# Performance work log

Measured on AMD Instinct MI355X. Metric: run time of the kernel, lower is better.

The kernel has to match this reference:

```python
import jax, jax.numpy as jnp
import numpy as np

HEADS = 8
DIM_HEAD = 64


def setup_inputs() -> dict:
    key = jax.random.key(0)
    k1, k2, k3 = jax.random.split(key, 3)
    B, F, N_PATCH, DIM = 8, 16, 196, 512
    seq = 1 + F * N_PATCH  # 3137
    inner = HEADS * DIM_HEAD  # 512
    x = jax.random.normal(k1, (B, seq, DIM), dtype=jnp.float32)
    Wqkv = jax.random.normal(k2, (DIM, 3 * inner), dtype=jnp.float32) * (DIM ** -0.5)
    Wout = jax.random.normal(k3, (inner, DIM), dtype=jnp.float32) * (inner ** -0.5)
    bout = jnp.zeros((DIM,), dtype=jnp.float32)
    return {"x": x, "Wqkv": Wqkv, "Wout": Wout, "bout": bout, "f": F}


def _attn(q, k, v):
    # q: [b, i, d], k/v: [b, j, d]
    sim = jnp.einsum('bid,bjd->bij', q, k)
    a = jax.nn.softmax(sim, axis=-1)
    return jnp.einsum('bij,bjd->bid', a, v)


def reference(x, Wqkv, Wout, bout, f):
    B, N, D = x.shape
    h, dh = HEADS, DIM_HEAD
    scale = dh ** -0.5
    qkv = x @ Wqkv  # [B, N, 3*h*dh]
    q, k, v = jnp.split(qkv, 3, axis=-1)

    def to_bh(t):  # 'b n (h d) -> (b h) n d'
        return t.reshape(B, N, h, dh).transpose(0, 2, 1, 3).reshape(B * h, N, dh)

    q, k, v = to_bh(q), to_bh(k), to_bh(v)
    q = q * scale

    cls_q, q_ = q[:, :1], q[:, 1:]
    cls_k, k_ = k[:, :1], k[:, 1:]
    cls_v, v_ = v[:, :1], v[:, 1:]

    # cls token attends to all tokens
    cls_out = _attn(cls_q, k, v)  # [(b h), 1, dh]

    n = (N - 1) // f
    # 'b (f n) d -> (b f) n d'
    def split_frames(t):
        return t.reshape(B * h, f, n, dh).reshape(B * h * f, n, dh)

    q_, k_, v_ = split_frames(q_), split_frames(k_), split_frames(v_)

    # 'b () d -> (b r) () d' with r = f
    cls_k = jnp.repeat(cls_k, f, axis=0)
    cls_v = jnp.repeat(cls_v, f, axis=0)
    k_ = jnp.concatenate((cls_k, k_), axis=1)  # [(b h f), n+1, dh]
    v_ = jnp.concatenate((cls_v, v_), axis=1)

    out = _attn(q_, k_, v_)  # [(b h f), n, dh]
    out = out.reshape(B * h, f * n, dh)  # '(b f) n d -> b (f n) d'
    out = jnp.concatenate((cls_out, out), axis=1)  # [(b h), N, dh]
    # '(b h) n d -> b n (h d)'
    out = out.reshape(B, h, N, dh).transpose(0, 2, 1, 3).reshape(B, N, h * dh)
    return out @ Wout + bout
```

## Files before the change

kernel.cpp:

```cpp
#include <hip/hip_runtime.h>
#include <hip/hip_bf16.h>

#define B_    8
#define F_    16
#define NP_   196
#define SEQ_  3137
#define H_    8
#define DH_   64
#define BH_   64
#define M_    25096
#define MPAD_ 25216
#define DIM_  512
#define NQKV_ 1536
#define NCH_  13

typedef _Float16 half8_t __attribute__((ext_vector_type(8)));
typedef _Float16 half4_t __attribute__((ext_vector_type(4)));
typedef float f32x4 __attribute__((ext_vector_type(4)));

#define XH_OFF     ((size_t)0)
#define WQKVT_OFF  ((size_t)25821184)
#define WOUTT_OFF  ((size_t)27394048)
#define QH_OFF     ((size_t)27918336)
#define KH_OFF     ((size_t)53616640)
#define VH_OFF     ((size_t)79314944)
#define ATTNH_OFF  ((size_t)105013248)
#define CLSP_OFF   XH_OFF

__device__ __forceinline__ void load_lds16(const _Float16* g, _Float16* l) {
  __builtin_amdgcn_global_load_lds(
      (const __attribute__((address_space(1))) void*)g,
      (__attribute__((address_space(3))) void*)l, 16, 0, 0);
}

__device__ __forceinline__ int xcd_swz(int orig, int nwg) {
  int q = nwg >> 3, r = nwg & 7;
  int x = orig & 7, j = orig >> 3;
  return (x < r ? x * (q + 1) : r * (q + 1) + (x - r) * q) + j;
}

__global__ __launch_bounds__(256) void convert_x_kernel(
    const float* __restrict__ x, _Float16* __restrict__ xh) {
  const size_t n8 = (size_t)M_ * DIM_ / 8;
  for (size_t i = (size_t)blockIdx.x * blockDim.x + threadIdx.x; i < n8;
       i += (size_t)gridDim.x * blockDim.x) {
    float4 a = ((const float4*)x)[2 * i];
    float4 b = ((const float4*)x)[2 * i + 1];
    half8_t h;
    h[0] = (_Float16)a.x; h[1] = (_Float16)a.y; h[2] = (_Float16)a.z; h[3] = (_Float16)a.w;
    h[4] = (_Float16)b.x; h[5] = (_Float16)b.y; h[6] = (_Float16)b.z; h[7] = (_Float16)b.w;
    ((half8_t*)xh)[i] = h;
  }
}

__global__ __launch_bounds__(256) void transpose_conv2_kernel(
    const float* __restrict__ wqkv, _Float16* __restrict__ wqkvT,
    const float* __restrict__ wout, _Float16* __restrict__ woutT) {
  __shared__ float tile[32][33];
  int by = blockIdx.y;
  const float* in; _Float16* out; int C;
  if (by < 48) { in = wqkv; out = wqkvT; C = NQKV_; }
  else         { in = wout; out = woutT; C = DIM_;  by -= 48; }
  const int r0 = blockIdx.x * 32, c0 = by * 32;
  const int lr = threadIdx.x >> 5, lc = threadIdx.x & 31;
#pragma unroll
  for (int p = 0; p < 4; ++p) {
    int r = p * 8 + lr;
    tile[r][lc] = in[(size_t)(r0 + r) * C + c0 + lc];
  }
  __syncthreads();
#pragma unroll
  for (int p = 0; p < 4; ++p) {
    int rr = p * 8 + lr;
    out[(size_t)(c0 + rr) * DIM_ + r0 + lc] = (_Float16)tile[lc][rr];
  }
}

__device__ __forceinline__ void gemm_mainloop_f16(
    const _Float16* __restrict__ A, const _Float16* __restrict__ Bt,
    int m0, int n0, _Float16* As, _Float16* Bs, f32x4 acc[4][4]) {
  const int tid = threadIdx.x;
  const int w = tid >> 6, lane = tid & 63;
  const int wr = w >> 1, wc = w & 1;
  const int lrow = lane & 15;
  const int g = lane >> 4;
  const int sw = lane & 7;

  const int srow = lane >> 3;
  const int scol = ((lane & 7) ^ srow) << 3;

  for (int k0 = 0; k0 < DIM_; k0 += 64) {
#pragma unroll
    for (int i = 0; i < 4; ++i) {
      int c = w * 4 + i;
      int r = c * 8 + srow;
      load_lds16(A + (size_t)(m0 + r) * DIM_ + k0 + scol, As + c * 512);
      load_lds16(Bt + (size_t)(n0 + r) * DIM_ + k0 + scol, Bs + c * 512);
    }
    __syncthreads();

#pragma unroll
    for (int kk = 0; kk < 2; ++kk) {
      const int kf = ((kk * 4 + g) ^ sw) << 3;
      half8_t a[4], b[4];
#pragma unroll
      for (int m = 0; m < 4; ++m)
        a[m] = *(const half8_t*)(As + (wr * 64 + m * 16 + lrow) * 64 + kf);
#pragma unroll
      for (int n = 0; n < 4; ++n)
        b[n] = *(const half8_t*)(Bs + (wc * 64 + n * 16 + lrow) * 64 + kf);
#pragma unroll
      for (int m = 0; m < 4; ++m)
#pragma unroll
        for (int n = 0; n < 4; ++n)
          acc[m][n] = __builtin_amdgcn_mfma_f32_16x16x32_f16(a[m], b[n], acc[m][n], 0, 0, 0);
    }
    __syncthreads();
  }
}

__global__ __launch_bounds__(256) void qkv_gemm_kernel(
    const _Float16* __restrict__ xh, const _Float16* __restrict__ wqkvT,
    _Float16* __restrict__ qh, _Float16* __restrict__ kh, _Float16* __restrict__ vh) {
  __shared__ _Float16 As[128 * 64];
  __shared__ _Float16 Bs[128 * 64];
  const int nwg = 197 * 12;
  const int lin = xcd_swz(blockIdx.x, nwg);
  const int mb = lin / 12, nb = lin - mb * 12;
  const int m0 = mb * 128, n0 = nb * 128;

  f32x4 acc[4][4];
#pragma unroll
  for (int m = 0; m < 4; ++m)
#pragma unroll
    for (int n = 0; n < 4; ++n) acc[m][n] = (f32x4)0.f;

  gemm_mainloop_f16(xh, wqkvT, m0, n0, As, Bs, acc);

  const int tid = threadIdx.x;
  const int w = tid >> 6, lane = tid & 63;
  const int wr = w >> 1, wc = w & 1;
  const int g = lane >> 4, lrow = lane & 15;

  _Float16* stg = (w < 2) ? (As + w * 4096) : (Bs + (w - 2) * 4096);
  const int gcb0 = n0 + wc * 64;
  const int which = gcb0 >> 9;
  const int h = (gcb0 >> 6) & 7;
  const float scale = (which == 0) ? 0.125f : 1.0f;
  _Float16* dst = (which == 0) ? qh : (which == 1) ? kh : vh;

#pragma unroll
  for (int m = 0; m < 4; ++m)
#pragma unroll
    for (int n = 0; n < 4; ++n)
#pragma unroll
      for (int j = 0; j < 4; ++j) {
        int row = m * 16 + g * 4 + j;
        int col = n * 16 + lrow;
        int slot = (col >> 3) ^ (row & 7);
        stg[row * 64 + slot * 8 + (col & 7)] = (_Float16)(acc[m][n][j] * scale);
      }
  asm volatile("s_waitcnt lgkmcnt(0)" ::: "memory");
  __builtin_amdgcn_sched_barrier(0);

  const int rl = lane >> 3, cs = lane & 7;
#pragma unroll
  for (int rr = 0; rr < 8; ++rr) {
    int row = rr * 8 + rl;
    int grow = m0 + wr * 64 + row;
    if (grow < M_) {
      int b = grow / SEQ_;
      int t = grow - b * SEQ_;
      half8_t v = *(const half8_t*)(stg + row * 64 + ((cs ^ (row & 7)) << 3));
      *(half8_t*)(dst + ((size_t)(b * H_ + h) * SEQ_ + t) * DH_ + cs * 8) = v;
    }
  }
}

__global__ __launch_bounds__(256) void out_gemm_kernel(
    const _Float16* __restrict__ attnh, const _Float16* __restrict__ woutT,
    const float* __restrict__ bias, float* __restrict__ out) {
  __shared__ _Float16 As[128 * 64];
  __shared__ _Float16 Bs[128 * 64];
  const int nwg = 197 * 4;
  const int lin = xcd_swz(blockIdx.x, nwg);
  const int mb = lin >> 2, nb = lin & 3;
  const int m0 = mb * 128, n0 = nb * 128;

  f32x4 acc[4][4];
#pragma unroll
  for (int m = 0; m < 4; ++m)
#pragma unroll
    for (int n = 0; n < 4; ++n) acc[m][n] = (f32x4)0.f;

  gemm_mainloop_f16(attnh, woutT, m0, n0, As, Bs, acc);

  const int tid = threadIdx.x;
  const int w = tid >> 6, lane = tid & 63;
  const int wr = w >> 1, wc = w & 1;
#pragma unroll
  for (int n = 0; n < 4; ++n) {
    const int gcol = n0 + wc * 64 + n * 16 + (lane & 15);
    const float bv = bias[gcol];
#pragma unroll
    for (int m = 0; m < 4; ++m)
#pragma unroll
      for (int j = 0; j < 4; ++j) {
        int grow = m0 + wr * 64 + m * 16 + (lane >> 4) * 4 + j;
        if (grow < M_) out[(size_t)grow * DIM_ + gcol] = acc[m][n][j] + bv;
      }
  }
}

__global__ __launch_bounds__(256) void attn_kernel(
    const _Float16* __restrict__ qh, const _Float16* __restrict__ kh,
    const _Float16* __restrict__ vh, _Float16* __restrict__ attnh,
    float* __restrict__ clsp) {
  __shared__ _Float16 SMEM[36864];
  const int bx = blockIdx.x;
  const int tid = threadIdx.x;

  if (bx >= BH_ * F_) {
    const int pb = bx - BH_ * F_;
    const int bh = pb / NCH_, ch = pb - bh * NCH_;
    const int j0 = ch * 256;
    const int nk = min(256, SEQ_ - j0);
    _Float16* Kc = SMEM;
    float* qs  = (float*)(SMEM + 16384);
    float* pp  = qs + 64;
    float* red = pp + 256;
    const size_t kbase = (size_t)bh * SEQ_ * DH_;

#pragma unroll
    for (int i = 0; i < 8; ++i) {
      int c = i * 256 + tid;
      int row = c >> 3, cg = c & 7;
      int grow = min(j0 + row, SEQ_ - 1);
      load_lds16(kh + kbase + (size_t)grow * DH_ + (((cg ^ (row & 7)) << 3)),
                 Kc + (i * 256 + (tid & 192)) * 8);
    }
    if (tid < 64) qs[tid] = (float)qh[kbase * 1 + (size_t)0 * DH_ + tid];
    __syncthreads();

    float sc;
    {
      float s = 0.f;
#pragma unroll
      for (int i = 0; i < 8; ++i) {
        half8_t kk = *(const half8_t*)(Kc + tid * 64 + (((i ^ (tid & 7)) << 3)));
#pragma unroll
        for (int u = 0; u < 8; ++u) s += qs[8 * i + u] * (float)kk[u];
      }
      sc = (tid < nk) ? s : -1e30f;
    }
    red[tid] = sc; __syncthreads();
    for (int st = 128; st > 0; st >>= 1) {
      if (tid < st) red[tid] = fmaxf(red[tid], red[tid + st]);
      __syncthreads();
    }
    const float m = red[0]; __syncthreads();

    float p = (tid < nk) ? __expf(sc - m) : 0.f;
    pp[tid] = p;
    red[tid] = p; __syncthreads();
    for (int st = 128; st > 0; st >>= 1) {
      if (tid < st) red[tid] += red[tid + st];
      __syncthreads();
    }
    const float l = red[0]; __syncthreads();

    const int d = tid & 63, grp = tid >> 6;
    float a = 0.f;
#pragma unroll 4
    for (int u = 0; u < 64; ++u) {
      int jj = grp * 64 + u;
      int jc = min(j0 + jj, SEQ_ - 1);
      a += pp[jj] * (float)vh[((size_t)bh * SEQ_ + jc) * DH_ + d];
    }
    red[tid] = a; __syncthreads();
    if (tid < 64) {
      float asum = red[tid] + red[64 + tid] + red[128 + tid] + red[192 + tid];
      float* P = clsp + (size_t)(bh * NCH_ + ch) * 72;
      P[tid] = asum;
      if (tid == 0) { P[64] = m; P[65] = l; }
    }
    return;
  }

  const int bh = bx >> 4, fi = bx & 15;
  const int b = bh >> 3, h = bh & 7;
  const int w = tid >> 6, lane = tid & 63;
  const int g = lane >> 4, lc = lane & 15;
  _Float16* KL = SMEM;
  _Float16* VT = SMEM + 13312;
  _Float16* Pb = SMEM + 28160;
  _Float16* tmp = Pb;
  _Float16* Pw = Pb + w * (16 * 136);

  const size_t base = (size_t)bh * SEQ_ * DH_;

  half8_t qb0[4], qb1[4];
#pragma unroll
  for (int it = 0; it < 4; ++it) {
    int qq = min((w + it * 4) * 16 + lc, NP_ - 1);
    const _Float16* qp = qh + base + (size_t)(1 + fi * NP_ + qq) * DH_ + g * 8;
    qb0[it] = *(const half8_t*)(qp);
    qb1[it] = *(const half8_t*)(qp + 32);
  }

  for (int i = 0; i < 7; ++i) {
    int gran = i * 256 + tid;
    if (gran < 1664) {
      int row = gran >> 3, cg = gran & 7;
      int rowtok = (row == 0) ? 0 : fi * NP_ + min(row, NP_);
      load_lds16(kh + base + (size_t)rowtok * DH_ + ((cg ^ (row & 7)) << 3),
                 KL + (i * 256 + (tid & 192)) * 8);
    }
  }

#pragma unroll
  for (int half = 0; half < 2; ++half) {
    const int r0 = half * 104;
#pragma unroll
    for (int i = 0; i < 4; ++i) {
      int c = i * 256 + tid;
      if (c < 832) {
        int row = c >> 3, cg = c & 7;
        int gr = r0 + row;
        int rowtok = (gr == 0) ? 0 : fi * NP_ + min(gr, NP_);
        load_lds16(vh + base + (size_t)rowtok * DH_ + ((cg ^ (row & 7)) << 3),
                   tmp + (i * 256 + (tid & 192)) * 8);
      }
    }
    if (half == 1) {
      for (int idx = tid; idx < 64 * 35; idx += 256) {
        int d = idx / 35;
        VT[d * 232 + 197 + (idx - d * 35)] = (_Float16)0.f;
      }
    }
    __syncthreads();
#pragma unroll
    for (int i = 0; i < 4; ++i) {
      int item = i * 256 + tid;
      if (item < 832) {
        int cg = item / 104;
        int key = item - cg * 104;
        int gk = r0 + key;
        if (gk <= 196) {
          half8_t v = *(const half8_t*)(tmp + key * 64 + ((cg ^ (key & 7)) << 3));
#pragma unroll
          for (int u = 0; u < 8; ++u) VT[(cg * 8 + u) * 232 + gk] = v[u];
        }
      }
    }
    __syncthreads();
  }

  const f32x4 zero4 = (f32x4)0.f;

#pragma unroll
  for (int it = 0; it < 4; ++it) {
    const int qt = w + it * 4;
    if (qt < 13) {
      f32x4 st[13];
#pragma unroll
      for (int t = 0; t < 13; ++t) {
        int key = t * 16 + lc;
        const _Float16* kp = KL + key * 64;
        half8_t ka0 = *(const half8_t*)(kp + ((g ^ (key & 7)) << 3));
        half8_t ka1 = *(const half8_t*)(kp + (((4 + g) ^ (key & 7)) << 3));
        st[t] = __builtin_amdgcn_mfma_f32_16x16x32_f16(ka0, qb0[it], zero4, 0, 0, 0);
        st[t] = __builtin_amdgcn_mfma_f32_16x16x32_f16(ka1, qb1[it], st[t], 0, 0, 0);
      }

      float mx = -1e30f;
#pragma unroll
      for (int t = 0; t < 13; ++t)
#pragma unroll
        for (int j = 0; j < 4; ++j) {
          int key = t * 16 + g * 4 + j;
          if (key >= 197) st[t][j] = -1e30f;
          mx = fmaxf(mx, st[t][j]);
        }
      mx = fmaxf(mx, __shfl_xor(mx, 16));
      mx = fmaxf(mx, __shfl_xor(mx, 32));
      float l = 0.f;
#pragma unroll
      for (int t = 0; t < 13; ++t)
#pragma unroll
        for (int j = 0; j < 4; ++j) {
          float p = __expf(st[t][j] - mx);
          st[t][j] = p;
          l += p;
        }
      l += __shfl_xor(l, 16);
      l += __shfl_xor(l, 32);
      const float inv = 1.f / l;

      f32x4 o[4];
#pragma unroll
      for (int dt = 0; dt < 4; ++dt) o[dt] = zero4;

#pragma unroll
      for (int t = 0; t < 8; ++t) {
        half4_t hp;
#pragma unroll
        for (int j = 0; j < 4; ++j) hp[j] = (_Float16)(st[t][j] * inv);
        *(half4_t*)(Pw + lc * 136 + t * 16 + g * 4) = hp;
      }
#pragma unroll
      for (int c = 0; c < 4; ++c) {
        half8_t pa = *(const half8_t*)(Pw + lc * 136 + c * 32 + g * 8);
#pragma unroll
        for (int dt = 0; dt < 4; ++dt) {
          half8_t vb = *(const half8_t*)(VT + (dt * 16 + lc) * 232 + c * 32 + g * 8);
          o[dt] = __builtin_amdgcn_mfma_f32_16x16x32_f16(pa, vb, o[dt], 0, 0, 0);
        }
      }

#pragma unroll
      for (int t = 8; t < 13; ++t) {
        half4_t hp;
#pragma unroll
        for (int j = 0; j < 4; ++j) hp[j] = (_Float16)(st[t][j] * inv);
        *(half4_t*)(Pw + lc * 104 + (t - 8) * 16 + g * 4) = hp;
      }
      {
        half4_t hz;
#pragma unroll
        for (int j = 0; j < 4; ++j) hz[j] = (_Float16)0.f;
        *(half4_t*)(Pw + lc * 104 + 80 + g * 4) = hz;
      }
#pragma unroll
      for (int c = 4; c < 7; ++c) {
        half8_t pa = *(const half8_t*)(Pw + lc * 104 + (c - 4) * 32 + g * 8);
#pragma unroll
        for (int dt = 0; dt < 4; ++dt) {
          half8_t vb = *(const half8_t*)(VT + (dt * 16 + lc) * 232 + c * 32 + g * 8);
          o[dt] = __builtin_amdgcn_mfma_f32_16x16x32_f16(pa, vb, o[dt], 0, 0, 0);
        }
      }

#pragma unroll
      for (int dt = 0; dt < 4; ++dt)
#pragma unroll
        for (int j = 0; j < 4; ++j) {
          int q = qt * 16 + g * 4 + j;
          if (q < NP_) {
            int tok = 1 + fi * NP_ + q;
            attnh[((size_t)(b * SEQ_) + tok) * DIM_ + h * DH_ + dt * 16 + lc] =
                (_Float16)o[dt][j];
          }
        }
    }
  }
}

__global__ __launch_bounds__(64) void cls_combine_kernel(
    const float* __restrict__ clsp, _Float16* __restrict__ attnh) {
  const int bh = blockIdx.x;
  const int b = bh >> 3, h = bh & 7;
  const int d = threadIdx.x;
  const float* P = clsp + (size_t)bh * NCH_ * 72;

  float m = -1e30f;
#pragma unroll
  for (int c = 0; c < NCH_; ++c) m = fmaxf(m, P[c * 72 + 64]);
  float l = 0.f, o = 0.f;
#pragma unroll
  for (int c = 0; c < NCH_; ++c) {
    float wgt = __expf(P[c * 72 + 64] - m);
    l += P[c * 72 + 65] * wgt;
    o += P[c * 72 + d] * wgt;
  }
  attnh[(size_t)(b * SEQ_) * DIM_ + h * DH_ + d] = (_Float16)(o / l);
}

extern "C" void kernel_launch(void* const* d_in, const int* in_sizes, int n_in,
                              void* d_out, int out_size, void* d_ws, size_t ws_size,
                              hipStream_t stream) {
  (void)in_sizes; (void)n_in; (void)out_size; (void)ws_size;
  const float* x    = (const float*)d_in[0];
  const float* wqkv = (const float*)d_in[1];
  const float* wout = (const float*)d_in[2];
  const float* bout = (const float*)d_in[3];
  char* ws = (char*)d_ws;
  _Float16* xh    = (_Float16*)(ws + XH_OFF);
  _Float16* wqkvT = (_Float16*)(ws + WQKVT_OFF);
  _Float16* woutT = (_Float16*)(ws + WOUTT_OFF);
  _Float16* qh    = (_Float16*)(ws + QH_OFF);
  _Float16* kh    = (_Float16*)(ws + KH_OFF);
  _Float16* vh    = (_Float16*)(ws + VH_OFF);
  _Float16* attnh = (_Float16*)(ws + ATTNH_OFF);
  float*    clsp  = (float*)(ws + CLSP_OFF);
  float* out = (float*)d_out;

  convert_x_kernel<<<2048, 256, 0, stream>>>(x, xh);
  {
    dim3 g(16, 64);
    transpose_conv2_kernel<<<g, 256, 0, stream>>>(wqkv, wqkvT, wout, woutT);
  }

  qkv_gemm_kernel<<<197 * 12, 256, 0, stream>>>(xh, wqkvT, qh, kh, vh);

  attn_kernel<<<BH_ * F_ + BH_ * NCH_, 256, 0, stream>>>(qh, kh, vh, attnh, clsp);
  cls_combine_kernel<<<BH_, 64, 0, stream>>>(clsp, attnh);

  out_gemm_kernel<<<197 * 4, 256, 0, stream>>>(attnh, woutT, bout, out);
}
```

Before: 170.5 us.

## Fold CLS-token partial attention into per-frame attention blocks reusing staged K/V

```diff
diff --git a/kernel.cpp b/kernel.cpp
--- a/kernel.cpp
+++ b/kernel.cpp
@@ -12,7 +12,6 @@
 #define MPAD_ 25216
 #define DIM_  512
 #define NQKV_ 1536
-#define NCH_  13
 
 typedef _Float16 half8_t __attribute__((ext_vector_type(8)));
 typedef _Float16 half4_t __attribute__((ext_vector_type(4)));
@@ -220,73 +219,6 @@
   const int bx = blockIdx.x;
   const int tid = threadIdx.x;
 
-  if (bx >= BH_ * F_) {
-    const int pb = bx - BH_ * F_;
-    const int bh = pb / NCH_, ch = pb - bh * NCH_;
-    const int j0 = ch * 256;
-    const int nk = min(256, SEQ_ - j0);
-    _Float16* Kc = SMEM;
-    float* qs  = (float*)(SMEM + 16384);
-    float* pp  = qs + 64;
-    float* red = pp + 256;
-    const size_t kbase = (size_t)bh * SEQ_ * DH_;
-
-#pragma unroll
-    for (int i = 0; i < 8; ++i) {
-      int c = i * 256 + tid;
-      int row = c >> 3, cg = c & 7;
-      int grow = min(j0 + row, SEQ_ - 1);
-      load_lds16(kh + kbase + (size_t)grow * DH_ + (((cg ^ (row & 7)) << 3)),
-                 Kc + (i * 256 + (tid & 192)) * 8);
-    }
-    if (tid < 64) qs[tid] = (float)qh[kbase * 1 + (size_t)0 * DH_ + tid];
-    __syncthreads();
-
-    float sc;
-    {
-      float s = 0.f;
-#pragma unroll
-      for (int i = 0; i < 8; ++i) {
-        half8_t kk = *(const half8_t*)(Kc + tid * 64 + (((i ^ (tid & 7)) << 3)));
-#pragma unroll
-        for (int u = 0; u < 8; ++u) s += qs[8 * i + u] * (float)kk[u];
-      }
-      sc = (tid < nk) ? s : -1e30f;
-    }
-    red[tid] = sc; __syncthreads();
-    for (int st = 128; st > 0; st >>= 1) {
-      if (tid < st) red[tid] = fmaxf(red[tid], red[tid + st]);
-      __syncthreads();
-    }
-    const float m = red[0]; __syncthreads();
-
-    float p = (tid < nk) ? __expf(sc - m) : 0.f;
-    pp[tid] = p;
-    red[tid] = p; __syncthreads();
-    for (int st = 128; st > 0; st >>= 1) {
-      if (tid < st) red[tid] += red[tid + st];
-      __syncthreads();
-    }
-    const float l = red[0]; __syncthreads();
-
-    const int d = tid & 63, grp = tid >> 6;
-    float a = 0.f;
-#pragma unroll 4
-    for (int u = 0; u < 64; ++u) {
-      int jj = grp * 64 + u;
-      int jc = min(j0 + jj, SEQ_ - 1);
-      a += pp[jj] * (float)vh[((size_t)bh * SEQ_ + jc) * DH_ + d];
-    }
-    red[tid] = a; __syncthreads();
-    if (tid < 64) {
-      float asum = red[tid] + red[64 + tid] + red[128 + tid] + red[192 + tid];
-      float* P = clsp + (size_t)(bh * NCH_ + ch) * 72;
-      P[tid] = asum;
-      if (tid == 0) { P[64] = m; P[65] = l; }
-    }
-    return;
-  }
-
   const int bh = bx >> 4, fi = bx & 15;
   const int b = bh >> 3, h = bh & 7;
   const int w = tid >> 6, lane = tid & 63;
@@ -454,6 +386,56 @@
         }
     }
   }
+
+  __syncthreads();
+  float* qs  = (float*)Pb;
+  float* pp  = qs + 64;
+  float* red = pp + 256;
+  if (tid < 64) qs[tid] = (float)qh[base + tid];
+  __syncthreads();
+
+  const int kmin = (fi == 0) ? 0 : 1;
+  float sc = -1e30f;
+  if (tid >= kmin && tid < 197) {
+    float s = 0.f;
+#pragma unroll
+    for (int i = 0; i < 8; ++i) {
+      half8_t kk = *(const half8_t*)(KL + tid * 64 + ((i ^ (tid & 7)) << 3));
+#pragma unroll
+      for (int u = 0; u < 8; ++u) s += qs[8 * i + u] * (float)kk[u];
+    }
+    sc = s;
+  }
+  red[tid] = sc; __syncthreads();
+  for (int st = 128; st > 0; st >>= 1) {
+    if (tid < st) red[tid] = fmaxf(red[tid], red[tid + st]);
+    __syncthreads();
+  }
+  const float cm = red[0]; __syncthreads();
+
+  float cp = (tid >= kmin && tid < 197) ? __expf(sc - cm) : 0.f;
+  pp[tid] = cp;
+  red[tid] = cp; __syncthreads();
+  for (int st = 128; st > 0; st >>= 1) {
+    if (tid < st) red[tid] += red[tid + st];
+    __syncthreads();
+  }
+  const float clsum = red[0]; __syncthreads();
+
+  const int d = tid & 63;
+  float a = 0.f;
+#pragma unroll 4
+  for (int u = 0; u < 64; ++u) {
+    int k = w * 64 + u;
+    if (k <= 196) a += pp[k] * (float)VT[d * 232 + k];
+  }
+  red[tid] = a; __syncthreads();
+  if (tid < 64) {
+    float asum = red[tid] + red[64 + tid] + red[128 + tid] + red[192 + tid];
+    float* P = clsp + (size_t)(bh * 16 + fi) * 72;
+    P[tid] = asum;
+    if (tid == 0) { P[64] = cm; P[65] = clsum; }
+  }
 }
 
 __global__ __launch_bounds__(64) void cls_combine_kernel(
@@ -461,14 +443,14 @@
   const int bh = blockIdx.x;
   const int b = bh >> 3, h = bh & 7;
   const int d = threadIdx.x;
-  const float* P = clsp + (size_t)bh * NCH_ * 72;
+  const float* P = clsp + (size_t)bh * 16 * 72;
 
   float m = -1e30f;
 #pragma unroll
-  for (int c = 0; c < NCH_; ++c) m = fmaxf(m, P[c * 72 + 64]);
+  for (int c = 0; c < 16; ++c) m = fmaxf(m, P[c * 72 + 64]);
   float l = 0.f, o = 0.f;
 #pragma unroll
-  for (int c = 0; c < NCH_; ++c) {
+  for (int c = 0; c < 16; ++c) {
     float wgt = __expf(P[c * 72 + 64] - m);
     l += P[c * 72 + 65] * wgt;
     o += P[c * 72 + d] * wgt;
@@ -503,7 +485,7 @@
 
   qkv_gemm_kernel<<<197 * 12, 256, 0, stream>>>(xh, wqkvT, qh, kh, vh);
 
-  attn_kernel<<<BH_ * F_ + BH_ * NCH_, 256, 0, stream>>>(qh, kh, vh, attnh, clsp);
+  attn_kernel<<<BH_ * F_, 256, 0, stream>>>(qh, kh, vh, attnh, clsp);
   cls_combine_kernel<<<BH_, 64, 0, stream>>>(clsp, attnh);
 
   out_gemm_kernel<<<197 * 4, 256, 0, stream>>>(attnh, woutT, bout, out);
```

Measured after the change: 166.4 us. 1.02x faster.
